# Kernel optimization log

Hardware: AMD Instinct MI355X
Metric: run time of the kernel (lower is better)

Reference implementation:

```python
import jax, jax.numpy as jnp
import numpy as np

B, T, C, NH = 4, 2048, 1024, 16
HD = C // NH  # head dim = 64


def setup_inputs() -> dict:
    key = jax.random.key(0)
    k1, k2, k3 = jax.random.split(key, 3)
    x = jax.random.normal(k1, (B, T, C), dtype=jnp.float32)
    w_attn = jax.random.normal(k2, (C, 3 * C), dtype=jnp.float32) * (1.0 / np.sqrt(C))
    b_attn = jnp.zeros((3 * C,), dtype=jnp.float32)
    w_proj = jax.random.normal(k3, (C, C), dtype=jnp.float32) * (1.0 / np.sqrt(C))
    b_proj = jnp.zeros((C,), dtype=jnp.float32)
    return {"x": x, "w_attn": w_attn, "b_attn": b_attn, "w_proj": w_proj, "b_proj": b_proj}


def reference(x, w_attn, b_attn, w_proj, b_proj):
    Bx, Tx, Cx = x.shape
    # fused QKV projection
    qkv = x @ w_attn + b_attn              # [B, T, 3C]
    q, k, v = jnp.split(qkv, 3, axis=-1)   # each [B, T, C]
    # split heads: [B, NH, T, HD]
    q = q.reshape(Bx, Tx, NH, HD).transpose(0, 2, 1, 3)
    k = k.reshape(Bx, Tx, NH, HD).transpose(0, 2, 1, 3)
    v = v.reshape(Bx, Tx, NH, HD).transpose(0, 2, 1, 3)
    scale = 1.0 / np.sqrt(HD)
    att = jnp.einsum('bhqd,bhkd->bhqk', q, k) * scale  # [B, NH, T, T]
    causal = jnp.tril(jnp.ones((Tx, Tx), dtype=bool))
    att = jnp.where(causal[None, None], att, -jnp.inf)
    att = jax.nn.softmax(att, axis=-1)
    y = jnp.einsum('bhqk,bhkd->bhqd', att, v)           # [B, NH, T, HD]
    y = y.transpose(0, 2, 1, 3).reshape(Bx, Tx, Cx)
    return y @ w_proj + b_proj
```

## Files before the change

kernel.cpp:

```cpp
#include <hip/hip_runtime.h>
#include <hip/hip_bf16.h>

#define B_SZ 4
#define T_SZ 2048
#define C_SZ 1024
#define NH_SZ 16
#define HD_SZ 64
#define M_SZ (B_SZ * T_SZ)

typedef __bf16 bf16x8 __attribute__((ext_vector_type(8)));
typedef __bf16 bf16x4 __attribute__((ext_vector_type(4)));
typedef float f32x4 __attribute__((ext_vector_type(4)));

__device__ __forceinline__ void store_out(float* p, float v) { *p = v; }
__device__ __forceinline__ void store_out(__hip_bfloat16* p, float v) { *p = __float2bfloat16(v); }

__device__ __forceinline__ void async_ld16(__hip_bfloat16* lds, const __hip_bfloat16* g) {
  __builtin_amdgcn_global_load_lds(
      (const __attribute__((address_space(1))) void*)g,
      (__attribute__((address_space(3))) void*)lds, 16, 0, 0);
}

__global__ __launch_bounds__(256) void conv_bf16_kernel(
    const float* __restrict__ X, __hip_bfloat16* __restrict__ Y) {
  const int i = (blockIdx.x * 256 + threadIdx.x) * 4;
  float4 v = *(const float4*)&X[i];
  union { bf16x4 v; __hip_bfloat16 h[4]; } o;
  o.h[0] = __float2bfloat16(v.x); o.h[1] = __float2bfloat16(v.y);
  o.h[2] = __float2bfloat16(v.z); o.h[3] = __float2bfloat16(v.w);
  *(bf16x4*)&Y[i] = o.v;
}

template <int KD, int ND>
__global__ __launch_bounds__(256) void transpose_conv_kernel(
    const float* __restrict__ W, __hip_bfloat16* __restrict__ Wt) {
  __shared__ float sT[32][33];
  const int n0 = blockIdx.x * 32, k0 = blockIdx.y * 32;
  const int tid = threadIdx.x;
  {
    const int r = tid >> 3, c = (tid & 7) * 4;
    float4 v = *(const float4*)&W[(size_t)(k0 + r) * ND + n0 + c];
    sT[r][c] = v.x; sT[r][c + 1] = v.y; sT[r][c + 2] = v.z; sT[r][c + 3] = v.w;
  }
  __syncthreads();
  {
    const int n = tid >> 3, kq = (tid & 7) * 4;
    union { bf16x4 v; __hip_bfloat16 h[4]; } o;
#pragma unroll
    for (int j = 0; j < 4; ++j) o.h[j] = __float2bfloat16(sT[kq + j][n]);
    *(bf16x4*)&Wt[(size_t)(n0 + n) * KD + k0 + kq] = o.v;
  }
}

template <int N, int K, bool SPLIT, typename OutT>
__global__ __launch_bounds__(256) void gemm_glds_kernel(
    const __hip_bfloat16* __restrict__ A, const __hip_bfloat16* __restrict__ Bt,
    const float* __restrict__ bias, OutT* __restrict__ C,
    __hip_bfloat16* __restrict__ qR, __hip_bfloat16* __restrict__ kR,
    __hip_bfloat16* __restrict__ vT) {
  __shared__ __align__(16) __hip_bfloat16 sA[128 * 32];
  __shared__ __align__(16) __hip_bfloat16 sB[128 * 32];

  const int tid = threadIdx.x;
  const int wave = tid >> 6, lane = tid & 63;
  const int quad = lane >> 4, l16 = lane & 15;
  const int bm = blockIdx.y * 128, bn = blockIdx.x * 128;

  f32x4 acc[4][4];
#pragma unroll
  for (int i = 0; i < 4; ++i)
#pragma unroll
    for (int j = 0; j < 4; ++j) acc[i][j] = (f32x4){0.f, 0.f, 0.f, 0.f};

  const int grow = wave * 32 + (lane >> 2);
  const int gcol = (lane & 3) * 8;
  const int lb0 = (wave * 32) * 32 + lane * 8;
  const int lb1 = (wave * 32 + 16) * 32 + lane * 8;
  const int rw = (wave & 1) * 64, cw = (wave >> 1) * 64;

  for (int k0 = 0; k0 < K; k0 += 32) {
    __syncthreads();
    async_ld16(&sA[lb0], A + (size_t)(bm + grow) * K + k0 + gcol);
    async_ld16(&sA[lb1], A + (size_t)(bm + grow + 16) * K + k0 + gcol);
    async_ld16(&sB[lb0], Bt + (size_t)(bn + grow) * K + k0 + gcol);
    async_ld16(&sB[lb1], Bt + (size_t)(bn + grow + 16) * K + k0 + gcol);
    __syncthreads();

    bf16x8 af[4], bfr[4];
#pragma unroll
    for (int i = 0; i < 4; ++i)
      af[i] = *(const bf16x8*)&sA[(rw + i * 16 + l16) * 32 + quad * 8];
#pragma unroll
    for (int j = 0; j < 4; ++j)
      bfr[j] = *(const bf16x8*)&sB[(cw + j * 16 + l16) * 32 + quad * 8];
#pragma unroll
    for (int i = 0; i < 4; ++i)
#pragma unroll
      for (int j = 0; j < 4; ++j)
        acc[i][j] = __builtin_amdgcn_mfma_f32_16x16x32_bf16(af[i], bfr[j], acc[i][j], 0, 0, 0);
  }

#pragma unroll
  for (int i = 0; i < 4; ++i)
#pragma unroll
    for (int j = 0; j < 4; ++j) {
      const int col = bn + cw + j * 16 + l16;
      const float bv = bias[col];
#pragma unroll
      for (int r = 0; r < 4; ++r) {
        const int row = bm + rw + i * 16 + quad * 4 + r;
        const float val = acc[i][j][r] + bv;
        if (SPLIT) {
          const int bb = row >> 11, t = row & 2047;
          const int hh = (col >> 6) & 15, d = col & 63;
          const int bh64 = bb * 16 + hh;
          if (col < C_SZ) {
            qR[((size_t)bh64 * T_SZ + t) * HD_SZ + d] = __float2bfloat16(val * 0.125f);
          } else if (col < 2 * C_SZ) {
            kR[((size_t)bh64 * T_SZ + t) * HD_SZ + d] = __float2bfloat16(val);
          } else {
            vT[((size_t)bh64 * HD_SZ + d) * T_SZ + t] = __float2bfloat16(val);
          }
        } else {
          store_out(&C[(size_t)row * N + col], val);
        }
      }
    }
}

#define ATT_ST 72

__global__ __launch_bounds__(256, 4) void attn_mfma_kernel(
    const __hip_bfloat16* __restrict__ qR, const __hip_bfloat16* __restrict__ kR,
    const __hip_bfloat16* __restrict__ vT, __hip_bfloat16* __restrict__ y) {
  __shared__ __align__(16) __hip_bfloat16 sQ[64][ATT_ST];
  __shared__ __align__(16) __hip_bfloat16 sK[64][ATT_ST];
  __shared__ __align__(16) __hip_bfloat16 sVt[64][ATT_ST];
  __shared__ __align__(16) __hip_bfloat16 sP[64][ATT_ST];

  const int bh = blockIdx.x;
  const int tile = (int)gridDim.y - 1 - blockIdx.y;
  const int t0 = tile * 64;
  const int tid = threadIdx.x;
  const int wave = tid >> 6, lane = tid & 63;
  const int quad = lane >> 4, l16 = lane & 15;
  const int wrow0 = wave * 16;

  const __hip_bfloat16* qb = qR + (size_t)bh * T_SZ * HD_SZ;
  const __hip_bfloat16* kb = kR + (size_t)bh * T_SZ * HD_SZ;
  const __hip_bfloat16* vb = vT + (size_t)bh * HD_SZ * T_SZ;

  const int sr = tid >> 2, sc = (tid & 3) * 16;

  {
    const __hip_bfloat16* src = qb + (size_t)t0 * HD_SZ + tid * 16;
    *(float4*)&sQ[sr][sc] = *(const float4*)src;
    *(float4*)&sQ[sr][sc + 8] = *(const float4*)(src + 8);
  }

  float4 krg0, krg1, vrg0, vrg1;
  {
    const __hip_bfloat16* ks = kb + tid * 16;
    krg0 = *(const float4*)ks;
    krg1 = *(const float4*)(ks + 8);
    const __hip_bfloat16* vs = vb + (size_t)sr * T_SZ + sc;
    vrg0 = *(const float4*)vs;
    vrg1 = *(const float4*)(vs + 8);
  }

  __syncthreads();
  bf16x8 qa0 = *(const bf16x8*)&sQ[wrow0 + l16][quad * 8];
  bf16x8 qa1 = *(const bf16x8*)&sQ[wrow0 + l16][32 + quad * 8];

  float lp[4];
  f32x4 o[4];
#pragma unroll
  for (int r = 0; r < 4; ++r) lp[r] = 0.f;
#pragma unroll
  for (int nn = 0; nn < 4; ++nn) o[nn] = (f32x4){0.f, 0.f, 0.f, 0.f};

  for (int j0 = 0; j0 <= t0; j0 += 64) {
    *(float4*)&sK[sr][sc] = krg0;
    *(float4*)&sK[sr][sc + 8] = krg1;
    *(float4*)&sVt[sr][sc] = vrg0;
    *(float4*)&sVt[sr][sc + 8] = vrg1;
    if (j0 + 64 <= t0) {
      const __hip_bfloat16* ks = kb + (size_t)(j0 + 64) * HD_SZ + tid * 16;
      krg0 = *(const float4*)ks;
      krg1 = *(const float4*)(ks + 8);
      const __hip_bfloat16* vs = vb + (size_t)sr * T_SZ + j0 + 64 + sc;
      vrg0 = *(const float4*)vs;
      vrg1 = *(const float4*)(vs + 8);
    }
    __syncthreads();

    f32x4 s[4];
#pragma unroll
    for (int sub = 0; sub < 4; ++sub) {
      s[sub] = (f32x4){0.f, 0.f, 0.f, 0.f};
      bf16x8 kf0 = *(const bf16x8*)&sK[sub * 16 + l16][quad * 8];
      s[sub] = __builtin_amdgcn_mfma_f32_16x16x32_bf16(qa0, kf0, s[sub], 0, 0, 0);
      bf16x8 kf1 = *(const bf16x8*)&sK[sub * 16 + l16][32 + quad * 8];
      s[sub] = __builtin_amdgcn_mfma_f32_16x16x32_bf16(qa1, kf1, s[sub], 0, 0, 0);
    }

    if (j0 == t0) {
#pragma unroll
      for (int sub = 0; sub < 4; ++sub) {
        const int key_l = sub * 16 + l16;
#pragma unroll
        for (int r = 0; r < 4; ++r) {
          const int row_l = wrow0 + quad * 4 + r;
          if (key_l > row_l) s[sub][r] = -1e30f;
        }
      }
    }

#pragma unroll
    for (int sub = 0; sub < 4; ++sub)
#pragma unroll
      for (int r = 0; r < 4; ++r) s[sub][r] = __expf(s[sub][r]);
#pragma unroll
    for (int r = 0; r < 4; ++r)
      lp[r] += (s[0][r] + s[1][r]) + (s[2][r] + s[3][r]);

#pragma unroll
    for (int sub = 0; sub < 4; ++sub)
#pragma unroll
      for (int r = 0; r < 4; ++r)
        sP[wrow0 + quad * 4 + r][sub * 16 + l16] = __float2bfloat16(s[sub][r]);

    bf16x8 pa0 = *(const bf16x8*)&sP[wrow0 + l16][quad * 8];
    bf16x8 pa1 = *(const bf16x8*)&sP[wrow0 + l16][32 + quad * 8];

#pragma unroll
    for (int nn = 0; nn < 4; ++nn) {
      bf16x8 vf0 = *(const bf16x8*)&sVt[nn * 16 + l16][quad * 8];
      o[nn] = __builtin_amdgcn_mfma_f32_16x16x32_bf16(pa0, vf0, o[nn], 0, 0, 0);
      bf16x8 vf1 = *(const bf16x8*)&sVt[nn * 16 + l16][32 + quad * 8];
      o[nn] = __builtin_amdgcn_mfma_f32_16x16x32_bf16(pa1, vf1, o[nn], 0, 0, 0);
    }

    if (j0 < t0) __syncthreads();
  }

#pragma unroll
  for (int off = 1; off <= 8; off <<= 1)
#pragma unroll
    for (int r = 0; r < 4; ++r) lp[r] += __shfl_xor(lp[r], off);
  float inv[4];
#pragma unroll
  for (int r = 0; r < 4; ++r) inv[r] = 1.0f / lp[r];

  const int b = bh >> 4, h = bh & 15;
#pragma unroll
  for (int nn = 0; nn < 4; ++nn)
#pragma unroll
    for (int r = 0; r < 4; ++r) {
      const int t = t0 + wrow0 + quad * 4 + r;
      y[((size_t)b * T_SZ + t) * C_SZ + h * HD_SZ + nn * 16 + l16] =
          __float2bfloat16(o[nn][r] * inv[r]);
    }
}

extern "C" void kernel_launch(void* const* d_in, const int* in_sizes, int n_in,
                              void* d_out, int out_size, void* d_ws, size_t ws_size,
                              hipStream_t stream) {
  const float* x      = (const float*)d_in[0];
  const float* w_attn = (const float*)d_in[1];
  const float* b_attn = (const float*)d_in[2];
  const float* w_proj = (const float*)d_in[3];
  const float* b_proj = (const float*)d_in[4];
  float* out = (float*)d_out;

  __hip_bfloat16* xb  = (__hip_bfloat16*)d_ws;
  __hip_bfloat16* waT = xb + (size_t)M_SZ * C_SZ;
  __hip_bfloat16* wpT = waT + (size_t)3 * C_SZ * C_SZ;
  __hip_bfloat16* qR  = wpT + (size_t)C_SZ * C_SZ;
  __hip_bfloat16* kR  = qR + (size_t)M_SZ * C_SZ;
  __hip_bfloat16* vT  = kR + (size_t)M_SZ * C_SZ;
  __hip_bfloat16* yb  = xb;

  conv_bf16_kernel<<<(M_SZ * C_SZ) / (256 * 4), 256, 0, stream>>>(x, xb);
  transpose_conv_kernel<C_SZ, 3 * C_SZ><<<dim3(96, 32), 256, 0, stream>>>(w_attn, waT);
  transpose_conv_kernel<C_SZ, C_SZ><<<dim3(32, 32), 256, 0, stream>>>(w_proj, wpT);

  gemm_glds_kernel<3 * C_SZ, C_SZ, true, __hip_bfloat16>
      <<<dim3(24, 64), 256, 0, stream>>>(xb, waT, b_attn, nullptr, qR, kR, vT);

  attn_mfma_kernel<<<dim3(B_SZ * NH_SZ, T_SZ / 64), 256, 0, stream>>>(qR, kR, vT, yb);

  gemm_glds_kernel<C_SZ, C_SZ, false, float>
      <<<dim3(8, 64), 256, 0, stream>>>(yb, wpT, b_proj, out, nullptr, nullptr, nullptr);
}
```

Before: 284.4 us.

## Add 256x256-tile double-buffered QKV GEMM with swizzled LDS and block remap

Replaces the QKV projection GEMM with a new kernel that uses 512 threads per block, 256x256 output tiles and double-buffered async global-to-LDS loads. It XOR-swizzles the LDS layout to avoid bank conflicts and remaps block IDs to improve cache locality. MFMA phases are raised in priority with s_setprio. The larger tile raises data reuse per byte loaded. In exchange, 384 blocks on the GPU's CUs can leave a partial tail wave, and the 128KB of LDS limits occupancy to one block per CU.

```diff
diff --git a/kernel.cpp b/kernel.cpp
--- a/kernel.cpp
+++ b/kernel.cpp
@@ -19,6 +19,12 @@
   __builtin_amdgcn_global_load_lds(
       (const __attribute__((address_space(1))) void*)g,
       (__attribute__((address_space(3))) void*)lds, 16, 0, 0);
+}
+
+__device__ __forceinline__ void bar() {
+  asm volatile("" ::: "memory");
+  __builtin_amdgcn_s_barrier();
+  asm volatile("" ::: "memory");
 }
 
 __global__ __launch_bounds__(256) void conv_bf16_kernel(
@@ -128,6 +134,130 @@
     }
 }
 
+__device__ __forceinline__ bf16x8 lds_frag(const __hip_bfloat16* base, int row,
+                                           int kk, int quad) {
+  const int byte = row * 128 + (((kk << 6) | (quad << 4)) ^ ((row & 7) << 4));
+  return *(const bf16x8*)((const char*)base + byte);
+}
+
+__global__ __launch_bounds__(512, 2) void gemm256_qkv_kernel(
+    const __hip_bfloat16* __restrict__ A, const __hip_bfloat16* __restrict__ Bt,
+    const float* __restrict__ bias,
+    __hip_bfloat16* __restrict__ qR, __hip_bfloat16* __restrict__ kR,
+    __hip_bfloat16* __restrict__ vT) {
+  __shared__ __align__(16) __hip_bfloat16 sA[2][256 * 64];
+  __shared__ __align__(16) __hip_bfloat16 sB[2][256 * 64];
+
+  const int tid = threadIdx.x;
+  const int wave = tid >> 6, lane = tid & 63;
+  const int quad = lane >> 4, l16 = lane & 15;
+  const int wm = wave >> 2, wn = wave & 3;
+
+  const int id = (blockIdx.x & 7) * 48 + (blockIdx.x >> 3);
+  const int bm = (id / 12) * 256;
+  const int bn = (id % 12) * 256;
+
+  const int srow = tid >> 3;
+  const int scol = ((((tid & 7) << 4) ^ ((srow & 7) << 4)) >> 1);
+  const int sdst = tid * 8;
+  const __hip_bfloat16* gA = A + (size_t)(bm + srow) * C_SZ + scol;
+  const __hip_bfloat16* gB = Bt + (size_t)(bn + srow) * C_SZ + scol;
+
+  f32x4 acc[8][4];
+#pragma unroll
+  for (int m = 0; m < 8; ++m)
+#pragma unroll
+    for (int n = 0; n < 4; ++n) acc[m][n] = (f32x4){0.f, 0.f, 0.f, 0.f};
+
+#define STAGE256(buf, kt)                                                     \
+  do {                                                                        \
+    _Pragma("unroll") for (int ii = 0; ii < 4; ++ii) {                        \
+      async_ld16(&sA[buf][ii * 4096 + sdst], gA + (size_t)ii * 64 * C_SZ + (kt) * 64); \
+      async_ld16(&sB[buf][ii * 4096 + sdst], gB + (size_t)ii * 64 * C_SZ + (kt) * 64); \
+    }                                                                         \
+  } while (0)
+
+  STAGE256(0, 0);
+  STAGE256(1, 1);
+  asm volatile("s_waitcnt vmcnt(8)" ::: "memory");
+  bar();
+
+  const int NT = C_SZ / 64;
+  for (int kt = 0; kt < NT; ++kt) {
+    const __hip_bfloat16* a_base = sA[kt & 1];
+    const __hip_bfloat16* b_base = sB[kt & 1];
+    bf16x8 af[4][2], bfr[2][2];
+
+#pragma unroll
+    for (int mh = 0; mh < 2; ++mh) {
+#pragma unroll
+      for (int mq = 0; mq < 4; ++mq)
+#pragma unroll
+        for (int kk = 0; kk < 2; ++kk)
+          af[mq][kk] = lds_frag(a_base, wm * 128 + mh * 64 + mq * 16 + l16, kk, quad);
+#pragma unroll
+      for (int nh = 0; nh < 2; ++nh) {
+#pragma unroll
+        for (int nq = 0; nq < 2; ++nq)
+#pragma unroll
+          for (int kk = 0; kk < 2; ++kk)
+            bfr[nq][kk] = lds_frag(b_base, wn * 64 + nh * 32 + nq * 16 + l16, kk, quad);
+        asm volatile("s_waitcnt lgkmcnt(0)" ::: "memory");
+        __builtin_amdgcn_sched_barrier(0);
+        __builtin_amdgcn_s_setprio(1);
+#pragma unroll
+        for (int mq = 0; mq < 4; ++mq)
+#pragma unroll
+          for (int nq = 0; nq < 2; ++nq)
+#pragma unroll
+            for (int kk = 0; kk < 2; ++kk)
+              acc[mh * 4 + mq][nh * 2 + nq] = __builtin_amdgcn_mfma_f32_16x16x32_bf16(
+                  af[mq][kk], bfr[nq][kk], acc[mh * 4 + mq][nh * 2 + nq], 0, 0, 0);
+        __builtin_amdgcn_s_setprio(0);
+      }
+    }
+
+    bar();
+    if (kt < NT - 2) {
+      STAGE256(kt & 1, kt + 2);
+      asm volatile("s_waitcnt vmcnt(8)" ::: "memory");
+      bar();
+    } else if (kt == NT - 2) {
+      asm volatile("s_waitcnt vmcnt(0)" ::: "memory");
+      bar();
+    }
+  }
+#undef STAGE256
+
+  float bv[4];
+#pragma unroll
+  for (int n = 0; n < 4; ++n) bv[n] = bias[bn + wn * 64 + n * 16 + l16];
+
+  const bool isQ = bn < C_SZ;
+  const bool isK = !isQ && bn < 2 * C_SZ;
+#pragma unroll
+  for (int m = 0; m < 8; ++m)
+#pragma unroll
+    for (int n = 0; n < 4; ++n) {
+      const int col = bn + wn * 64 + n * 16 + l16;
+      const int hh = (col >> 6) & 15, d = col & 63;
+#pragma unroll
+      for (int r = 0; r < 4; ++r) {
+        const int row = bm + wm * 128 + m * 16 + quad * 4 + r;
+        const int bb = row >> 11, t = row & 2047;
+        const int bh64 = bb * 16 + hh;
+        const float val = acc[m][n][r] + bv[n];
+        if (isQ) {
+          qR[((size_t)bh64 * T_SZ + t) * HD_SZ + d] = __float2bfloat16(val * 0.125f);
+        } else if (isK) {
+          kR[((size_t)bh64 * T_SZ + t) * HD_SZ + d] = __float2bfloat16(val);
+        } else {
+          vT[((size_t)bh64 * HD_SZ + d) * T_SZ + t] = __float2bfloat16(val);
+        }
+      }
+    }
+}
+
 #define ATT_ST 72
 
 __global__ __launch_bounds__(256, 4) void attn_mfma_kernel(
@@ -285,8 +415,7 @@
   transpose_conv_kernel<C_SZ, 3 * C_SZ><<<dim3(96, 32), 256, 0, stream>>>(w_attn, waT);
   transpose_conv_kernel<C_SZ, C_SZ><<<dim3(32, 32), 256, 0, stream>>>(w_proj, wpT);
 
-  gemm_glds_kernel<3 * C_SZ, C_SZ, true, __hip_bfloat16>
-      <<<dim3(24, 64), 256, 0, stream>>>(xb, waT, b_attn, nullptr, qR, kR, vT);
+  gemm256_qkv_kernel<<<dim3(384), 512, 0, stream>>>(xb, waT, b_attn, qR, kR, vT);
 
   attn_mfma_kernel<<<dim3(B_SZ * NH_SZ, T_SZ / 64), 256, 0, stream>>>(qR, kR, vT, yb);
 
```

Measured after the change: 294.7 us. 3.6% more time.

## Double-buffer GEMM LDS tiles with K=64 stages, XOR swizzle and block remap

Applied to the files above, without the earlier changes.

Rewrites both projection GEMMs to use double-buffered LDS tiles with a K-step of 64. The next tile is loaded via global_load_lds while MFMAs run on the current one, with one barrier per step instead of two. LDS rows are XOR-swizzled to avoid bank conflicts on fragment reads. The 2D grid is flattened and remapped across 8 groups (likely for XCD/L2 locality), and launch bounds request 2 blocks per CU. This doubles LDS use to 64KB per block, which may limit occupancy.

```diff
diff --git a/kernel.cpp b/kernel.cpp
--- a/kernel.cpp
+++ b/kernel.cpp
@@ -19,6 +19,12 @@
   __builtin_amdgcn_global_load_lds(
       (const __attribute__((address_space(1))) void*)g,
       (__attribute__((address_space(3))) void*)lds, 16, 0, 0);
+}
+
+__device__ __forceinline__ void bar() {
+  asm volatile("" ::: "memory");
+  __builtin_amdgcn_s_barrier();
+  asm volatile("" ::: "memory");
 }
 
 __global__ __launch_bounds__(256) void conv_bf16_kernel(
@@ -52,19 +58,36 @@
   }
 }
 
+__device__ __forceinline__ bf16x8 lds_frag(const __hip_bfloat16* base, int row,
+                                           int kk, int quad) {
+  const int byte = row * 128 + (((kk << 6) | (quad << 4)) ^ ((row & 7) << 4));
+  return *(const bf16x8*)((const char*)base + byte);
+}
+
 template <int N, int K, bool SPLIT, typename OutT>
-__global__ __launch_bounds__(256) void gemm_glds_kernel(
+__global__ __launch_bounds__(256, 2) void gemm_pipe_kernel(
     const __hip_bfloat16* __restrict__ A, const __hip_bfloat16* __restrict__ Bt,
     const float* __restrict__ bias, OutT* __restrict__ C,
     __hip_bfloat16* __restrict__ qR, __hip_bfloat16* __restrict__ kR,
     __hip_bfloat16* __restrict__ vT) {
-  __shared__ __align__(16) __hip_bfloat16 sA[128 * 32];
-  __shared__ __align__(16) __hip_bfloat16 sB[128 * 32];
+  __shared__ __align__(16) __hip_bfloat16 sA[2][128 * 64];
+  __shared__ __align__(16) __hip_bfloat16 sB[2][128 * 64];
 
   const int tid = threadIdx.x;
   const int wave = tid >> 6, lane = tid & 63;
   const int quad = lane >> 4, l16 = lane & 15;
-  const int bm = blockIdx.y * 128, bn = blockIdx.x * 128;
+  const int rw = (wave & 1) * 64, cw = (wave >> 1) * 64;
+
+  constexpr int NBN = N / 128;
+  constexpr int NBLK = (M_SZ / 128) * NBN;
+  const int id = ((int)blockIdx.x & 7) * (NBLK / 8) + ((int)blockIdx.x >> 3);
+  const int bm = (id / NBN) * 128, bn = (id % NBN) * 128;
+
+  const int srow = tid >> 3;
+  const int scol = ((((tid & 7) << 4) ^ ((srow & 7) << 4)) >> 1);
+  const int sdst = tid * 8;
+  const __hip_bfloat16* gA = A + (size_t)(bm + srow) * K + scol;
+  const __hip_bfloat16* gB = Bt + (size_t)(bn + srow) * K + scol;
 
   f32x4 acc[4][4];
 #pragma unroll
@@ -72,33 +95,48 @@
 #pragma unroll
     for (int j = 0; j < 4; ++j) acc[i][j] = (f32x4){0.f, 0.f, 0.f, 0.f};
 
-  const int grow = wave * 32 + (lane >> 2);
-  const int gcol = (lane & 3) * 8;
-  const int lb0 = (wave * 32) * 32 + lane * 8;
-  const int lb1 = (wave * 32 + 16) * 32 + lane * 8;
-  const int rw = (wave & 1) * 64, cw = (wave >> 1) * 64;
-
-  for (int k0 = 0; k0 < K; k0 += 32) {
-    __syncthreads();
-    async_ld16(&sA[lb0], A + (size_t)(bm + grow) * K + k0 + gcol);
-    async_ld16(&sA[lb1], A + (size_t)(bm + grow + 16) * K + k0 + gcol);
-    async_ld16(&sB[lb0], Bt + (size_t)(bn + grow) * K + k0 + gcol);
-    async_ld16(&sB[lb1], Bt + (size_t)(bn + grow + 16) * K + k0 + gcol);
-    __syncthreads();
-
-    bf16x8 af[4], bfr[4];
-#pragma unroll
-    for (int i = 0; i < 4; ++i)
-      af[i] = *(const bf16x8*)&sA[(rw + i * 16 + l16) * 32 + quad * 8];
-#pragma unroll
-    for (int j = 0; j < 4; ++j)
-      bfr[j] = *(const bf16x8*)&sB[(cw + j * 16 + l16) * 32 + quad * 8];
-#pragma unroll
-    for (int i = 0; i < 4; ++i)
-#pragma unroll
-      for (int j = 0; j < 4; ++j)
-        acc[i][j] = __builtin_amdgcn_mfma_f32_16x16x32_bf16(af[i], bfr[j], acc[i][j], 0, 0, 0);
-  }
+#define STG128(buf, kt)                                                        \
+  do {                                                                         \
+    _Pragma("unroll") for (int ii = 0; ii < 4; ++ii) {                         \
+      async_ld16(&sA[buf][ii * 2048 + sdst], gA + (size_t)(ii * 32) * K + (kt) * 64); \
+      async_ld16(&sB[buf][ii * 2048 + sdst], gB + (size_t)(ii * 32) * K + (kt) * 64); \
+    }                                                                          \
+  } while (0)
+
+  STG128(0, 0);
+  asm volatile("s_waitcnt vmcnt(0)" ::: "memory");
+  bar();
+
+  constexpr int NT = K / 64;
+  for (int kt = 0; kt < NT; ++kt) {
+    if (kt + 1 < NT) STG128((kt + 1) & 1, kt + 1);
+    const __hip_bfloat16* a_base = sA[kt & 1];
+    const __hip_bfloat16* b_base = sB[kt & 1];
+
+    bf16x8 af[4][2], bfr[4][2];
+#pragma unroll
+    for (int mq = 0; mq < 4; ++mq)
+#pragma unroll
+      for (int kk = 0; kk < 2; ++kk)
+        af[mq][kk] = lds_frag(a_base, rw + mq * 16 + l16, kk, quad);
+#pragma unroll
+    for (int nq = 0; nq < 4; ++nq)
+#pragma unroll
+      for (int kk = 0; kk < 2; ++kk)
+        bfr[nq][kk] = lds_frag(b_base, cw + nq * 16 + l16, kk, quad);
+#pragma unroll
+    for (int kk = 0; kk < 2; ++kk)
+#pragma unroll
+      for (int mq = 0; mq < 4; ++mq)
+#pragma unroll
+        for (int nq = 0; nq < 4; ++nq)
+          acc[mq][nq] = __builtin_amdgcn_mfma_f32_16x16x32_bf16(
+              af[mq][kk], bfr[nq][kk], acc[mq][nq], 0, 0, 0);
+
+    asm volatile("s_waitcnt vmcnt(0)" ::: "memory");
+    bar();
+  }
+#undef STG128
 
 #pragma unroll
   for (int i = 0; i < 4; ++i)
@@ -285,11 +323,11 @@
   transpose_conv_kernel<C_SZ, 3 * C_SZ><<<dim3(96, 32), 256, 0, stream>>>(w_attn, waT);
   transpose_conv_kernel<C_SZ, C_SZ><<<dim3(32, 32), 256, 0, stream>>>(w_proj, wpT);
 
-  gemm_glds_kernel<3 * C_SZ, C_SZ, true, __hip_bfloat16>
-      <<<dim3(24, 64), 256, 0, stream>>>(xb, waT, b_attn, nullptr, qR, kR, vT);
+  gemm_pipe_kernel<3 * C_SZ, C_SZ, true, __hip_bfloat16>
+      <<<dim3(1536), 256, 0, stream>>>(xb, waT, b_attn, nullptr, qR, kR, vT);
 
   attn_mfma_kernel<<<dim3(B_SZ * NH_SZ, T_SZ / 64), 256, 0, stream>>>(qR, kR, vT, yb);
 
-  gemm_glds_kernel<C_SZ, C_SZ, false, float>
-      <<<dim3(8, 64), 256, 0, stream>>>(yb, wpT, b_proj, out, nullptr, nullptr, nullptr);
-}
+  gemm_pipe_kernel<C_SZ, C_SZ, false, float>
+      <<<dim3(512), 256, 0, stream>>>(yb, wpT, b_proj, out, nullptr, nullptr, nullptr);
+}
```

Result: no change. 282.6 us (-0.6%).
